# Kernel optimization log

Measured on AMD Instinct MI355X. Metric: run time of the kernel, lower is better.

The kernel has to match this reference:

```python
import jax, jax.numpy as jnp
import numpy as np

IN_CHANNELS = 128
N_NODES = 100000
N_EDGES = 625000


def setup_inputs() -> dict:
    key = jax.random.key(0)
    k1, k2, k3, k4, k5, k6 = jax.random.split(key, 6)
    d = IN_CHANNELS
    x = jax.random.normal(k1, (N_NODES, d), dtype=jnp.float32)
    edge_index = jax.random.randint(k2, (2, N_EDGES), 0, N_NODES, dtype=jnp.int64)
    # Linear params, torch default init: U(-1/sqrt(fan_in), 1/sqrt(fan_in))
    b1_bound = 1.0 / np.sqrt(2 * d)
    W1 = jax.random.uniform(k3, (d, 2 * d), minval=-b1_bound, maxval=b1_bound, dtype=jnp.float32)
    b1 = jax.random.uniform(k4, (d,), minval=-b1_bound, maxval=b1_bound, dtype=jnp.float32)
    b2_bound = 1.0 / np.sqrt(d)
    W2 = jax.random.uniform(k5, (1, d), minval=-b2_bound, maxval=b2_bound, dtype=jnp.float32)
    b2 = jax.random.uniform(k6, (1,), minval=-b2_bound, maxval=b2_bound, dtype=jnp.float32)
    return {"x": x, "edge_index": edge_index, "W1": W1, "b1": b1, "W2": W2, "b2": b2}


def reference(x, edge_index, W1, b1, W2, b2):
    # Gather endpoint features and concat along feature dim: [E, 2d]
    h = jnp.concatenate([x[edge_index[0]], x[edge_index[1]]], axis=1)
    h = jax.nn.relu(h @ W1.T + b1)          # [E, d]
    h = jax.nn.relu(h @ W2.T + b2)          # [E, 1]
    return jax.nn.sigmoid(h)
```

## Files before the change

kernel.cpp:

```cpp
#include <hip/hip_runtime.h>
#include <hip/hip_bf16.h>
#include <hip/hip_fp16.h>
#include <math.h>


typedef short    s16x4 __attribute__((ext_vector_type(4)));
typedef short    s16x8 __attribute__((ext_vector_type(8)));
typedef float    f32x2 __attribute__((ext_vector_type(2)));
typedef float    f32x4 __attribute__((ext_vector_type(4)));
typedef unsigned u32x4 __attribute__((ext_vector_type(4)));
typedef _Float16 h16x2 __attribute__((ext_vector_type(2)));

#define D 128

static __device__ inline short f2bf(float f) {
    unsigned u = __builtin_bit_cast(unsigned, f);
    unsigned r = (u + 0x7FFFu + ((u >> 16) & 1u)) >> 16;
    return (short)r;
}

static __device__ inline unsigned pkbf16(float a, float b) {
    unsigned r;
    asm("v_cvt_pk_bf16_f32 %0, %1, %2" : "=v"(r) : "v"(a), "v"(b));
    return r;
}

static __device__ inline void stage16(const void* g, void* l) {
    __builtin_amdgcn_global_load_lds(
        (const __attribute__((address_space(1))) void*)g,
        (__attribute__((address_space(3))) void*)l, 16, 0, 0);
}

static __device__ inline unsigned enc1_sw(float f) {
    f = fminf(fmaxf(f, -448.f), 448.f);
    unsigned short h = __builtin_bit_cast(unsigned short, (_Float16)(f * (1.0f / 256.0f)));
    unsigned s = (h >> 8) & 0x80u;
    unsigned mag = h & 0x7FFFu;
    mag = mag + 0x3Fu + ((mag >> 7) & 1u);
    return s | ((mag >> 7) & 0x7Fu);
}
static __device__ inline unsigned enc2(float a, float b) {
#if __has_builtin(__builtin_amdgcn_cvt_pk_fp8_f32)
    return ((unsigned)__builtin_amdgcn_cvt_pk_fp8_f32(a, b, 0, false)) & 0xFFFFu;
#else
    return enc1_sw(a) | (enc1_sw(b) << 8);
#endif
}

#if __has_builtin(__builtin_amdgcn_cvt_pk_f16_fp8)
#define EDGE_PATH 0
#elif __has_builtin(__builtin_amdgcn_cvt_pk_f32_fp8)
#define EDGE_PATH 1
#else
#define EDGE_PATH 2
#endif

#if EDGE_PATH == 0
#define YSC 1.0f
static __device__ inline h16x2 dec2lo(unsigned v) {
    return __builtin_amdgcn_cvt_pk_f16_fp8((short)v);
}
static __device__ inline h16x2 dec2hi(unsigned v) {
    return __builtin_amdgcn_cvt_pk_f16_fp8((short)(v >> 16));
}
#elif EDGE_PATH == 1
static __device__ inline f32x2 d32lo(unsigned v) {
    return __builtin_amdgcn_cvt_pk_f32_fp8((int)v, false);
}
static __device__ inline f32x2 d32hi(unsigned v) {
    return __builtin_amdgcn_cvt_pk_f32_fp8((int)v, true);
}
#else
#define YSC 256.0f
static __device__ inline h16x2 dec2lo(unsigned v) {
    unsigned p = __builtin_amdgcn_perm(0u, v, 0x0C010C00u);
    unsigned h = ((p << 8) & 0x80008000u) | ((p << 7) & 0x3F803F80u);
    return __builtin_bit_cast(h16x2, h);
}
static __device__ inline h16x2 dec2hi(unsigned v) {
    unsigned p = __builtin_amdgcn_perm(0u, v, 0x0C030C02u);
    unsigned h = ((p << 8) & 0x80008000u) | ((p << 7) & 0x3F803F80u);
    return __builtin_bit_cast(h16x2, h);
}
#endif

#if EDGE_PATH != 1
static __device__ inline h16x2 reluh(h16x2 v) {
#if __has_builtin(__builtin_elementwise_max)
    h16x2 z = { (_Float16)0.0f, (_Float16)0.0f };
    return __builtin_elementwise_max(v, z);
#else
    unsigned u = __builtin_bit_cast(unsigned, v);
    unsigned m = ((u >> 15) & 0x00010001u) * 0xFFFFu;
    u &= ~m;
    return __builtin_bit_cast(h16x2, u);
#endif
}
static __device__ inline float dot2acc(h16x2 a, h16x2 b, float c) {
#if __has_builtin(__builtin_amdgcn_fdot2)
    return __builtin_amdgcn_fdot2(a, b, c, false);
#else
    return c + (float)a[0] * (float)b[0] + (float)a[1] * (float)b[1];
#endif
}
#endif

#define GRIDA 768

__global__ __launch_bounds__(256, 3) void precompute_kernel(
    const float* __restrict__ x,
    const float* __restrict__ W1,
    const float* __restrict__ b1,
    unsigned char* __restrict__ Y8,
    int N, int ntiles)
{
    __shared__ float Xt[2][32 * 128];

    const int tid  = threadIdx.x;
    const int wid  = tid >> 6;
    const int lane = tid & 63;
    const int quad = lane >> 4, l15 = lane & 15;
    const int cs   = wid;

    s16x8 bf[4][4];
    #pragma unroll
    for (int j = 0; j < 4; ++j) {
        #pragma unroll
        for (int c = 0; c < 4; ++c) {
            int o  = cs * 64 + j * 16 + l15;
            int kb = c * 32 + quad * 8;
            const float* wp = W1 + (size_t)(o & 127) * 256 + (o >> 7) * 128 + kb;
            float4 u0 = *(const float4*)wp;
            float4 u1 = *(const float4*)(wp + 4);
            bf[c][j] = (s16x8){ f2bf(u0.x), f2bf(u0.y), f2bf(u0.z), f2bf(u0.w),
                                f2bf(u1.x), f2bf(u1.y), f2bf(u1.z), f2bf(u1.w) };
        }
    }

    const int rl   = wid * 2 + (lane >> 5);
    const int colb = (lane & 31) * 16;
    const char* xbytes = (const char*)x;

    auto stage_tile = [&](int tt, int bb) {
        char* lb = (char*)&Xt[bb][0] + wid * 1024;
        #pragma unroll
        for (int i = 0; i < 4; ++i) {
            int row = i * 8 + rl;
            int m = tt * 32 + row; if (m >= N) m = N - 1;
            stage16(xbytes + (size_t)m * 512 + (colb ^ ((row & 7) << 4)),
                    lb + i * 4096);
        }
    };

    int t = blockIdx.x;
    if (t < ntiles) stage_tile(t, 0);

    const int swz = (l15 & 7) << 4;
    int buf = 0;
    while (t < ntiles) {
        const int tn = t + GRIDA;

        asm volatile("s_waitcnt vmcnt(0)" ::: "memory");
        __syncthreads();

        f32x4 acc[2][4];
        #pragma unroll
        for (int j = 0; j < 4; ++j) {
            f32x4 bi = (cs < 2) ? *(const f32x4*)&b1[cs * 64 + j * 16 + quad * 4]
                                : (f32x4){0.f, 0.f, 0.f, 0.f};
            acc[0][j] = bi; acc[1][j] = bi;
        }

        s16x8 af[2][4];
        {
            const char* xb8 = (const char*)&Xt[buf][0];
            #pragma unroll
            for (int i2 = 0; i2 < 2; ++i2) {
                const char* rp = xb8 + (i2 * 16 + l15) * 512;
                #pragma unroll
                for (int c = 0; c < 4; ++c) {
                    int kb = c * 128 + quad * 32;
                    f32x4 lo = *(const f32x4*)(rp + ( kb       ^ swz));
                    f32x4 hi = *(const f32x4*)(rp + ((kb + 16) ^ swz));
                    u32x4 pk;
                    pk[0] = pkbf16(lo[0], lo[1]);
                    pk[1] = pkbf16(lo[2], lo[3]);
                    pk[2] = pkbf16(hi[0], hi[1]);
                    pk[3] = pkbf16(hi[2], hi[3]);
                    af[i2][c] = __builtin_bit_cast(s16x8, pk);
                }
            }
        }

        if (tn < ntiles) stage_tile(tn, buf ^ 1);

        #pragma unroll
        for (int c = 0; c < 4; ++c)
            #pragma unroll
            for (int i2 = 0; i2 < 2; ++i2)
                #pragma unroll
                for (int j = 0; j < 4; ++j)
                    acc[i2][j] = __builtin_amdgcn_mfma_f32_16x16x32_bf16(
                        bf[c][j], af[i2][c], acc[i2][j], 0, 0, 0);

        const int m0 = t * 32;
        const bool qb0 = (quad & 1), qb1 = (quad & 2);
        #pragma unroll
        for (int i2 = 0; i2 < 2; ++i2) {
            unsigned dw[4];
            #pragma unroll
            for (int j = 0; j < 4; ++j) {
                f32x4 v = acc[i2][j];
                dw[j] = enc2(v[0], v[1]) | (enc2(v[2], v[3]) << 16);
            }
            unsigned s01 = qb0 ? dw[0] : dw[1];
            unsigned r01 = __shfl_xor(s01, 16);
            unsigned s23 = qb0 ? dw[2] : dw[3];
            unsigned r23 = __shfl_xor(s23, 16);
            unsigned a0 = qb0 ? r01 : dw[0];
            unsigned a1 = qb0 ? dw[1] : r01;
            unsigned a2 = qb0 ? r23 : dw[2];
            unsigned a3 = qb0 ? dw[3] : r23;
            unsigned s02 = qb1 ? a0 : a2;
            unsigned r02 = __shfl_xor(s02, 32);
            unsigned s13 = qb1 ? a1 : a3;
            unsigned r13 = __shfl_xor(s13, 32);
            uint4 ov;
            ov.x = qb1 ? r02 : a0;
            ov.y = qb1 ? r13 : a1;
            ov.z = qb1 ? a2 : r02;
            ov.w = qb1 ? a3 : r13;
            int m = m0 + i2 * 16 + l15;
            if (m < N)
                *(uint4*)(Y8 + (size_t)m * 256 + cs * 64 + quad * 16) = ov;
        }

        buf ^= 1;
        t = tn;
    }
}

#define EPB 256

__global__ __launch_bounds__(256, 4) void edge_kernel(
    const unsigned char* __restrict__ Y8,
    const int*           __restrict__ ei,
    const float*         __restrict__ W2,
    const float*         __restrict__ b2,
    float*               __restrict__ out,
    int E)
{
    __shared__ int eis[2][EPB];

    const int tid = threadIdx.x;
    const int sub = tid & 7;
    const int grp = tid >> 3;
    const int e0b = blockIdx.x * EPB;

    {
        int e = e0b + tid;
        eis[0][tid] = (e < E) ? ei[e] : 0;
        eis[1][tid] = (e < E) ? ei[(size_t)E + e] : 0;
    }
    __syncthreads();

#if EDGE_PATH == 1
    f32x2 w2f[8];
    {
        const float* wp = &W2[sub * 16];
        #pragma unroll
        for (int q = 0; q < 8; ++q)
            w2f[q] = *(const f32x2*)(wp + q * 2);
    }
#else
    h16x2 w2h[8];
    {
        const float* wp = &W2[sub * 16];
        #pragma unroll
        for (int q = 0; q < 8; ++q) {
            float2 f = *(const float2*)(wp + q * 2);
            w2h[q] = (h16x2){ (_Float16)(f.x * YSC), (_Float16)(f.y * YSC) };
        }
    }
#endif

    uint4 L[8], R[8];
    #pragma unroll
    for (int k = 0; k < 8; ++k) {
        int ib  = grp + 32 * k;
        int src = eis[0][ib];
        int dst = eis[1][ib];
        L[k] = *(const uint4*)(Y8 + (size_t)src * 256 + sub * 16);
        R[k] = *(const uint4*)(Y8 + (size_t)dst * 256 + 128 + sub * 16);
    }

    float s[8] = { 0.f, 0.f, 0.f, 0.f, 0.f, 0.f, 0.f, 0.f };
    #pragma unroll
    for (int k = 0; k < 8; ++k) {
        const unsigned* a = (const unsigned*)&L[k];
        const unsigned* c = (const unsigned*)&R[k];
        #pragma unroll
        for (int d = 0; d < 4; ++d) {
#if EDGE_PATH == 1
            f32x2 zl = d32lo(a[d]) + d32lo(c[d]);
            f32x2 zh = d32hi(a[d]) + d32hi(c[d]);
            s[k] = fmaf(fmaxf(zl[0], 0.f), w2f[2*d][0], s[k]);
            s[k] = fmaf(fmaxf(zl[1], 0.f), w2f[2*d][1], s[k]);
            s[k] = fmaf(fmaxf(zh[0], 0.f), w2f[2*d + 1][0], s[k]);
            s[k] = fmaf(fmaxf(zh[1], 0.f), w2f[2*d + 1][1], s[k]);
#else
            h16x2 za = reluh(dec2lo(a[d]) + dec2lo(c[d]));
            s[k] = dot2acc(za, w2h[2*d],     s[k]);
            h16x2 zb = reluh(dec2hi(a[d]) + dec2hi(c[d]));
            s[k] = dot2acc(zb, w2h[2*d + 1], s[k]);
#endif
        }
    }

    #pragma unroll
    for (int k = 0; k < 8; ++k) {
        s[k] += __shfl_xor(s[k], 1);
        s[k] += __shfl_xor(s[k], 2);
        s[k] += __shfl_xor(s[k], 4);
    }

    if (sub == 0) {
        float bb = b2[0];
        #pragma unroll
        for (int k = 0; k < 8; ++k) {
            int e = e0b + grp + 32 * k;
            if (e < E) {
                float t = fmaxf(s[k] + bb, 0.f);
                out[e] = 1.0f / (1.0f + expf(-t));
            }
        }
    }
}

#define BM   128
#define BK   64
#define LDT  72

__global__ __launch_bounds__(256) void decoder_fallback_kernel(
    const float* __restrict__ x, const int* __restrict__ ei,
    const float* __restrict__ W1, const float* __restrict__ b1,
    const float* __restrict__ W2, const float* __restrict__ b2,
    float* __restrict__ out, int E)
{
    __shared__ int   nid[2][BM];
    __shared__ short At[BM * LDT];
    __shared__ short Bt[D * LDT];
    __shared__ float rowsum[BM][2];

    const int tid = threadIdx.x;
    const int e0  = blockIdx.x * BM;
    if (tid < BM) { int e = e0 + tid; nid[0][tid] = (e < E) ? ei[e] : 0; }
    else { int e = e0 + (tid - BM); nid[1][tid - BM] = (e < E) ? ei[E + e] : 0; }

    const int wid = tid >> 6, lane = tid & 63;
    const int wm = wid >> 1, wn = wid & 1;
    const int quad = lane >> 4, l15 = lane & 15;
    const int srow = tid >> 4, scol = (tid & 15) * 4;
    f32x4 acc[4][4] = {};
    __syncthreads();

    for (int t = 0; t < 4; ++t) {
        const int* ids = nid[t >> 1];
        const int kx = (t & 1) * BK, kw = t * BK;
        #pragma unroll
        for (int p = 0; p < 8; ++p) {
            int row = srow + p * 16;
            float4 v = *(const float4*)&x[(size_t)ids[row] * D + kx + scol];
            s16x4 bv = { f2bf(v.x), f2bf(v.y), f2bf(v.z), f2bf(v.w) };
            *(s16x4*)&At[row * LDT + scol] = bv;
        }
        #pragma unroll
        for (int p = 0; p < 8; ++p) {
            int n = srow + p * 16;
            float4 v = *(const float4*)&W1[n * 256 + kw + scol];
            s16x4 bv = { f2bf(v.x), f2bf(v.y), f2bf(v.z), f2bf(v.w) };
            *(s16x4*)&Bt[n * LDT + scol] = bv;
        }
        __syncthreads();
        #pragma unroll
        for (int c = 0; c < 2; ++c) {
            const int kc = c * 32;
            s16x8 af[4], bfr[4];
            #pragma unroll
            for (int i = 0; i < 4; ++i)
                af[i] = *(const s16x8*)&At[(wm*64 + i*16 + l15) * LDT + kc + quad*8];
            #pragma unroll
            for (int j = 0; j < 4; ++j)
                bfr[j] = *(const s16x8*)&Bt[(wn*64 + j*16 + l15) * LDT + kc + quad*8];
            #pragma unroll
            for (int i = 0; i < 4; ++i)
                #pragma unroll
                for (int j = 0; j < 4; ++j)
                    acc[i][j] = __builtin_amdgcn_mfma_f32_16x16x32_bf16(
                        af[i], bfr[j], acc[i][j], 0, 0, 0);
        }
        __syncthreads();
    }
    float b1v[4], w2v[4];
    #pragma unroll
    for (int j = 0; j < 4; ++j) {
        int col = wn*64 + j*16 + l15;
        b1v[j] = b1[col]; w2v[j] = W2[col];
    }
    float psum[16];
    #pragma unroll
    for (int t = 0; t < 16; ++t) psum[t] = 0.f;
    #pragma unroll
    for (int i = 0; i < 4; ++i)
        #pragma unroll
        for (int j = 0; j < 4; ++j)
            #pragma unroll
            for (int r = 0; r < 4; ++r) {
                float c = fmaxf(acc[i][j][r] + b1v[j], 0.f);
                psum[i*4 + r] += c * w2v[j];
            }
    #pragma unroll
    for (int off = 1; off < 16; off <<= 1)
        #pragma unroll
        for (int t = 0; t < 16; ++t)
            psum[t] += __shfl_xor(psum[t], off);
    if (l15 == 0) {
        #pragma unroll
        for (int i = 0; i < 4; ++i)
            #pragma unroll
            for (int r = 0; r < 4; ++r)
                rowsum[wm*64 + i*16 + quad*4 + r][wn] = psum[i*4 + r];
    }
    __syncthreads();
    if (tid < BM) {
        int e = e0 + tid;
        if (e < E) {
            float s = rowsum[tid][0] + rowsum[tid][1] + b2[0];
            s = fmaxf(s, 0.f);
            out[e] = 1.0f / (1.0f + expf(-s));
        }
    }
}

extern "C" void kernel_launch(void* const* d_in, const int* in_sizes, int n_in,
                              void* d_out, int out_size, void* d_ws, size_t ws_size,
                              hipStream_t stream) {
    const float* x  = (const float*)d_in[0];
    const int*   ei = (const int*)d_in[1];
    const float* W1 = (const float*)d_in[2];
    const float* b1 = (const float*)d_in[3];
    const float* W2 = (const float*)d_in[4];
    const float* b2 = (const float*)d_in[5];
    float* out = (float*)d_out;

    int E = in_sizes[1] / 2;
    int N = in_sizes[0] / D;

    size_t y_bytes = (size_t)N * 256;
    if (ws_size >= y_bytes) {
        unsigned char* Y8 = (unsigned char*)d_ws;
        int ntiles = (N + 31) / 32;
        int gridA  = (ntiles < GRIDA) ? ntiles : GRIDA;
        precompute_kernel<<<gridA, 256, 0, stream>>>(x, W1, b1, Y8, N, ntiles);
        int gridB = (E + EPB - 1) / EPB;
        edge_kernel<<<gridB, 256, 0, stream>>>(Y8, ei, W2, b2, out, E);
    } else {
        int nblocks = (E + BM - 1) / BM;
        decoder_fallback_kernel<<<nblocks, 256, 0, stream>>>(
            x, ei, W1, b1, W2, b2, out, E);
    }
}
```

Before: 132.3 us.

## Load node features directly from global memory instead of LDS double-buffering

The precompute kernel drops the shared-memory double-buffered staging of x tiles (global_load_lds plus barriers) and instead has each wave read its bf16 fragments straight from global memory. All four waves now each load the full 32-row tile redundantly, relying on L1/L2 to absorb the duplicate reads. This removes barriers and LDS traffic but gives up the explicit prefetch overlap. Software fp8 fallbacks are replaced with inline-asm conversions, and the W1 conversion now uses the packed bf16 instruction.

Measured after the change: 152.2 us. +15.1%, slower.

```diff
diff --git a/kernel.cpp b/kernel.cpp
--- a/kernel.cpp
+++ b/kernel.cpp
@@ -25,37 +25,18 @@
     return r;
 }
 
-static __device__ inline void stage16(const void* g, void* l) {
-    __builtin_amdgcn_global_load_lds(
-        (const __attribute__((address_space(1))) void*)g,
-        (__attribute__((address_space(3))) void*)l, 16, 0, 0);
-}
-
-static __device__ inline unsigned enc1_sw(float f) {
-    f = fminf(fmaxf(f, -448.f), 448.f);
-    unsigned short h = __builtin_bit_cast(unsigned short, (_Float16)(f * (1.0f / 256.0f)));
-    unsigned s = (h >> 8) & 0x80u;
-    unsigned mag = h & 0x7FFFu;
-    mag = mag + 0x3Fu + ((mag >> 7) & 1u);
-    return s | ((mag >> 7) & 0x7Fu);
-}
 static __device__ inline unsigned enc2(float a, float b) {
 #if __has_builtin(__builtin_amdgcn_cvt_pk_fp8_f32)
     return ((unsigned)__builtin_amdgcn_cvt_pk_fp8_f32(a, b, 0, false)) & 0xFFFFu;
 #else
-    return enc1_sw(a) | (enc1_sw(b) << 8);
+    unsigned r;
+    asm("v_cvt_pk_fp8_f32 %0, %1, %2" : "=v"(r) : "v"(a), "v"(b));
+    return r & 0xFFFFu;
 #endif
 }
 
 #if __has_builtin(__builtin_amdgcn_cvt_pk_f16_fp8)
 #define EDGE_PATH 0
-#elif __has_builtin(__builtin_amdgcn_cvt_pk_f32_fp8)
-#define EDGE_PATH 1
-#else
-#define EDGE_PATH 2
-#endif
-
-#if EDGE_PATH == 0
 #define YSC 1.0f
 static __device__ inline h16x2 dec2lo(unsigned v) {
     return __builtin_amdgcn_cvt_pk_f16_fp8((short)v);
@@ -63,28 +44,6 @@
 static __device__ inline h16x2 dec2hi(unsigned v) {
     return __builtin_amdgcn_cvt_pk_f16_fp8((short)(v >> 16));
 }
-#elif EDGE_PATH == 1
-static __device__ inline f32x2 d32lo(unsigned v) {
-    return __builtin_amdgcn_cvt_pk_f32_fp8((int)v, false);
-}
-static __device__ inline f32x2 d32hi(unsigned v) {
-    return __builtin_amdgcn_cvt_pk_f32_fp8((int)v, true);
-}
-#else
-#define YSC 256.0f
-static __device__ inline h16x2 dec2lo(unsigned v) {
-    unsigned p = __builtin_amdgcn_perm(0u, v, 0x0C010C00u);
-    unsigned h = ((p << 8) & 0x80008000u) | ((p << 7) & 0x3F803F80u);
-    return __builtin_bit_cast(h16x2, h);
-}
-static __device__ inline h16x2 dec2hi(unsigned v) {
-    unsigned p = __builtin_amdgcn_perm(0u, v, 0x0C030C02u);
-    unsigned h = ((p << 8) & 0x80008000u) | ((p << 7) & 0x3F803F80u);
-    return __builtin_bit_cast(h16x2, h);
-}
-#endif
-
-#if EDGE_PATH != 1
 static __device__ inline h16x2 reluh(h16x2 v) {
 #if __has_builtin(__builtin_elementwise_max)
     h16x2 z = { (_Float16)0.0f, (_Float16)0.0f };
@@ -103,6 +62,28 @@
     return c + (float)a[0] * (float)b[0] + (float)a[1] * (float)b[1];
 #endif
 }
+#else
+#define EDGE_PATH 1
+#if __has_builtin(__builtin_amdgcn_cvt_pk_f32_fp8)
+static __device__ inline f32x2 d32lo(unsigned v) {
+    return __builtin_amdgcn_cvt_pk_f32_fp8((int)v, false);
+}
+static __device__ inline f32x2 d32hi(unsigned v) {
+    return __builtin_amdgcn_cvt_pk_f32_fp8((int)v, true);
+}
+#else
+static __device__ inline f32x2 d32lo(unsigned v) {
+    f32x2 r;
+    asm("v_cvt_pk_f32_fp8 %0, %1" : "=v"(r) : "v"(v));
+    return r;
+}
+static __device__ inline f32x2 d32hi(unsigned v) {
+    f32x2 r;
+    unsigned s = v >> 16;
+    asm("v_cvt_pk_f32_fp8 %0, %1" : "=v"(r) : "v"(s));
+    return r;
+}
+#endif
 #endif
 
 #define GRIDA 768
@@ -114,8 +95,6 @@
     unsigned char* __restrict__ Y8,
     int N, int ntiles)
 {
-    __shared__ float Xt[2][32 * 128];
-
     const int tid  = threadIdx.x;
     const int wid  = tid >> 6;
     const int lane = tid & 63;
@@ -130,38 +109,21 @@
             int o  = cs * 64 + j * 16 + l15;
             int kb = c * 32 + quad * 8;
             const float* wp = W1 + (size_t)(o & 127) * 256 + (o >> 7) * 128 + kb;
-            float4 u0 = *(const float4*)wp;
-            float4 u1 = *(const float4*)(wp + 4);
-            bf[c][j] = (s16x8){ f2bf(u0.x), f2bf(u0.y), f2bf(u0.z), f2bf(u0.w),
-                                f2bf(u1.x), f2bf(u1.y), f2bf(u1.z), f2bf(u1.w) };
-        }
-    }
-
-    const int rl   = wid * 2 + (lane >> 5);
-    const int colb = (lane & 31) * 16;
-    const char* xbytes = (const char*)x;
-
-    auto stage_tile = [&](int tt, int bb) {
-        char* lb = (char*)&Xt[bb][0] + wid * 1024;
-        #pragma unroll
-        for (int i = 0; i < 4; ++i) {
-            int row = i * 8 + rl;
-            int m = tt * 32 + row; if (m >= N) m = N - 1;
-            stage16(xbytes + (size_t)m * 512 + (colb ^ ((row & 7) << 4)),
-                    lb + i * 4096);
-        }
-    };
-
-    int t = blockIdx.x;
-    if (t < ntiles) stage_tile(t, 0);
-
-    const int swz = (l15 & 7) << 4;
-    int buf = 0;
-    while (t < ntiles) {
-        const int tn = t + GRIDA;
-
-        asm volatile("s_waitcnt vmcnt(0)" ::: "memory");
-        __syncthreads();
+            f32x4 u0 = *(const f32x4*)wp;
+            f32x4 u1 = *(const f32x4*)(wp + 4);
+            u32x4 pk;
+            pk[0] = pkbf16(u0[0], u0[1]);
+            pk[1] = pkbf16(u0[2], u0[3]);
+            pk[2] = pkbf16(u1[0], u1[1]);
+            pk[3] = pkbf16(u1[2], u1[3]);
+            bf[c][j] = __builtin_bit_cast(s16x8, pk);
+        }
+    }
+
+    const bool qb0 = (quad & 1), qb1 = (quad & 2);
+
+    for (int t = blockIdx.x; t < ntiles; t += GRIDA) {
+        const int m0 = t * 32;
 
         f32x4 acc[2][4];
         #pragma unroll
@@ -171,40 +133,30 @@
             acc[0][j] = bi; acc[1][j] = bi;
         }
 
-        s16x8 af[2][4];
-        {
-            const char* xb8 = (const char*)&Xt[buf][0];
-            #pragma unroll
-            for (int i2 = 0; i2 < 2; ++i2) {
-                const char* rp = xb8 + (i2 * 16 + l15) * 512;
-                #pragma unroll
-                for (int c = 0; c < 4; ++c) {
-                    int kb = c * 128 + quad * 32;
-                    f32x4 lo = *(const f32x4*)(rp + ( kb       ^ swz));
-                    f32x4 hi = *(const f32x4*)(rp + ((kb + 16) ^ swz));
-                    u32x4 pk;
-                    pk[0] = pkbf16(lo[0], lo[1]);
-                    pk[1] = pkbf16(lo[2], lo[3]);
-                    pk[2] = pkbf16(hi[0], hi[1]);
-                    pk[3] = pkbf16(hi[2], hi[3]);
-                    af[i2][c] = __builtin_bit_cast(s16x8, pk);
-                }
+        #pragma unroll
+        for (int i2 = 0; i2 < 2; ++i2) {
+            int m = m0 + i2 * 16 + l15; if (m >= N) m = N - 1;
+            const float* xr = x + (size_t)m * D + quad * 8;
+            s16x8 af[4];
+            #pragma unroll
+            for (int c = 0; c < 4; ++c) {
+                f32x4 lo = *(const f32x4*)(xr + c * 32);
+                f32x4 hi = *(const f32x4*)(xr + c * 32 + 4);
+                u32x4 pk;
+                pk[0] = pkbf16(lo[0], lo[1]);
+                pk[1] = pkbf16(lo[2], lo[3]);
+                pk[2] = pkbf16(hi[0], hi[1]);
+                pk[3] = pkbf16(hi[2], hi[3]);
+                af[c] = __builtin_bit_cast(s16x8, pk);
             }
-        }
-
-        if (tn < ntiles) stage_tile(tn, buf ^ 1);
-
-        #pragma unroll
-        for (int c = 0; c < 4; ++c)
-            #pragma unroll
-            for (int i2 = 0; i2 < 2; ++i2)
+            #pragma unroll
+            for (int c = 0; c < 4; ++c)
                 #pragma unroll
                 for (int j = 0; j < 4; ++j)
                     acc[i2][j] = __builtin_amdgcn_mfma_f32_16x16x32_bf16(
-                        bf[c][j], af[i2][c], acc[i2][j], 0, 0, 0);
-
-        const int m0 = t * 32;
-        const bool qb0 = (quad & 1), qb1 = (quad & 2);
+                        bf[c][j], af[c], acc[i2][j], 0, 0, 0);
+        }
+
         #pragma unroll
         for (int i2 = 0; i2 < 2; ++i2) {
             unsigned dw[4];
@@ -234,9 +186,6 @@
             if (m < N)
                 *(uint4*)(Y8 + (size_t)m * 256 + cs * 64 + quad * 16) = ov;
         }
-
-        buf ^= 1;
-        t = tn;
     }
 }
 
```
